# Kernel tuning notes

Hardware: AMD Instinct MI355X
Metric: run time of the kernel (lower is better)

## Reference

```python
import jax, jax.numpy as jnp
import numpy as np

B, T, H, NIN, D = 128, 64, 100, 3, 10


def _gru_cell(x, h, Wih, Whh, bih, bhh):
    # torch GRU cell: r,z,n gate ordering
    gi = x @ Wih.T + bih
    gh = h @ Whh.T + bhh
    ir, iz, inn = jnp.split(gi, 3, axis=-1)
    hr, hz, hn = jnp.split(gh, 3, axis=-1)
    r = jax.nn.sigmoid(ir + hr)
    z = jax.nn.sigmoid(iz + hz)
    n = jnp.tanh(inn + r * hn)
    return (1.0 - z) * n + z * h


def setup_inputs():
    keys = iter(jax.random.split(jax.random.key(0), 64))
    def rn(shape, scale):
        return jax.random.normal(next(keys), shape, dtype=jnp.float32) * scale
    inp = {"received": jax.random.normal(next(keys), (B, T, NIN), dtype=jnp.float32)}
    s = float(1.0 / np.sqrt(H))
    for p in ("w1", "w2"):
        inp[p + "_ih0"] = rn((3 * H, NIN), s)
        inp[p + "_hh0"] = rn((3 * H, H), s)
        inp[p + "_bih0"] = rn((3 * H,), s)
        inp[p + "_bhh0"] = rn((3 * H,), s)
        inp[p + "_ih1"] = rn((3 * H, H), s)
        inp[p + "_hh1"] = rn((3 * H, H), s)
        inp[p + "_bih1"] = rn((3 * H,), s)
        inp[p + "_bhh1"] = rn((3 * H,), s)
    s2 = float(1.0 / np.sqrt(2 * H))
    inp["attn_w"] = rn((1, 2 * H), s2)
    inp["attn_b"] = rn((1,), s2)
    inp["ctx_w"] = rn((H, 2 * H), s2)
    inp["ctx_b"] = rn((H,), s2)
    inp["out_w"] = rn((1, 2 * H), s2)
    inp["out_b"] = rn((1,), s2)
    return inp


def _forward(received, P1, P2, attn_w, attn_b, ctx_w, ctx_b, out_w, out_b):
    def two_layer(x, h, P):
        ih0, hh0, bih0, bhh0, ih1, hh1, bih1, bhh1 = P
        h0 = _gru_cell(x, h[0], ih0, hh0, bih0, bhh0)
        h1 = _gru_cell(h0, h[1], ih1, hh1, bih1, bhh1)
        # out = top-layer hidden; new hidden state [2,B,H]
        return h1, jnp.stack([h0, h1])

    def attend(hn, cache, t):
        # hn [2,B,H] (raw GRU hidden), cache [2,B,T,H] of past raw hiddens
        hrep = jnp.broadcast_to(hn[:, :, None, :], cache.shape)
        e = (jnp.concatenate([hrep, cache], axis=-1) @ attn_w.T)[..., 0] + attn_b[0]  # [2,B,T]
        mask = jnp.arange(T) < jnp.maximum(t, 1)  # safe mask (never all-False)
        a = jax.nn.softmax(jnp.where(mask, e, -1e30), axis=-1)
        c = jnp.einsum('lbt,lbth->lbh', a, cache)
        return jnp.concatenate([c, hn], axis=-1) @ ctx_w.T + ctx_b

    x_tm = jnp.transpose(received, (1, 0, 2))  # [T,B,NIN]
    h_init = jnp.zeros((2, B, H), jnp.float32)
    cache_init = jnp.zeros((2, B, T, H), jnp.float32)

    def step(carry, inp):
        h1, h2, c1, c2 = carry
        x, t = inp
        o1, h1n = two_layer(x, h1, P1)
        o2, h2n = two_layer(x, h2, P2)
        # attention over hiddens from steps 0..t-1 (cache updated AFTER attending)
        h1mix = attend(h1n, c1, t)
        h2mix = attend(h2n, c2, t)
        c1 = jax.lax.dynamic_update_slice(c1, h1n[:, :, None, :], (0, 0, t, 0))
        c2 = jax.lax.dynamic_update_slice(c2, h2n[:, :, None, :], (0, 0, t, 0))
        first = (t == 0)
        h1next = jnp.where(first, h1n, h1mix)
        h2next = jnp.where(first, h2n, h2mix)
        return (h1next, h2next, c1, c2), (o1, o2)

    _, (out1, out2) = jax.lax.scan(step, (h_init, h_init, cache_init, cache_init),
                                   (x_tm, jnp.arange(T)))
    out1 = jnp.transpose(out1, (1, 0, 2))  # [B,T,H]
    out2 = jnp.transpose(out2, (1, 0, 2))
    # readout: bit i pairs rnn_out1[i] with rnn_out2[min(i+D, T-1)]
    idx = jnp.minimum(jnp.arange(T) + D, T - 1)
    rnn_out = jnp.concatenate([out1, out2[:, idx, :]], axis=-1)  # [B,T,2H]
    logits = rnn_out @ out_w.T + out_b  # dec_act == 'linear'
    return jax.nn.sigmoid(logits)  # [B,T,1]


def reference(received, w1_ih0, w1_hh0, w1_bih0, w1_bhh0, w1_ih1, w1_hh1, w1_bih1, w1_bhh1,
              w2_ih0, w2_hh0, w2_bih0, w2_bhh0, w2_ih1, w2_hh1, w2_bih1, w2_bhh1,
              attn_w, attn_b, ctx_w, ctx_b, out_w, out_b):
    P1 = (w1_ih0, w1_hh0, w1_bih0, w1_bhh0, w1_ih1, w1_hh1, w1_bih1, w1_bhh1)
    P2 = (w2_ih0, w2_hh0, w2_bih0, w2_bhh0, w2_ih1, w2_hh1, w2_bih1, w2_bhh1)
    return _forward(received, P1, P2, attn_w, attn_b, ctx_w, ctx_b, out_w, out_b)
```

## Files before the change

kernel.cpp:

```cpp
#include <hip/hip_runtime.h>
#include <stdint.h>

#define H100 100
#define T64  64
#define NB   128
#define DLAG 10

#define OFF_HH0 0
#define OFF_IH1 30000
#define OFF_HH1 60000
#define OFF_CTX 90000
#define OFF_AWC 100000
#define OFF_OW  100050
#define OFF_P   100152

typedef _Float16 half2_t __attribute__((ext_vector_type(2)));
typedef __fp16   pk16x2  __attribute__((ext_vector_type(2)));

__device__ __forceinline__ float fdot2u(uint32_t a, uint32_t b, float c) {
#if __has_builtin(__builtin_amdgcn_fdot2)
    return __builtin_amdgcn_fdot2(__builtin_bit_cast(half2_t, a),
                                  __builtin_bit_cast(half2_t, b), c, false);
#else
    half2_t ha = __builtin_bit_cast(half2_t, a), hb = __builtin_bit_cast(half2_t, b);
    return c + (float)ha[0]*(float)hb[0] + (float)ha[1]*(float)hb[1];
#endif
}
__device__ __forceinline__ uint32_t pkrtz(float a, float b) {
    pk16x2 h = __builtin_amdgcn_cvt_pkrtz(a, b);
    return __builtin_bit_cast(uint32_t, h);
}
__device__ __forceinline__ uint32_t pk_rn(float a, float b) {
    half2_t h; h[0] = (_Float16)a; h[1] = (_Float16)b;
    return __builtin_bit_cast(uint32_t, h);
}
__device__ __forceinline__ float lo16(uint32_t u){ return (float)__builtin_bit_cast(half2_t,u)[0]; }
__device__ __forceinline__ float hi16(uint32_t u){ return (float)__builtin_bit_cast(half2_t,u)[1]; }
__device__ __forceinline__ float sigm(float x){ return 1.f/(1.f+__expf(-x)); }
__device__ __forceinline__ float tanhfast(float x){ return 1.f - 2.f/(1.f+__expf(2.f*x)); }
__device__ __forceinline__ float gru_el(float pr, float pz, float gin, float ghn, float hp) {
    float r = sigm(pr), z = sigm(pz);
    float n = tanhfast(gin + r*ghn);
    return (1.f - z)*n + z*hp;
}
__device__ __forceinline__ float wsum(float v){
    #pragma unroll
    for (int off = 32; off; off >>= 1) v += __shfl_xor(v, off);
    return v;
}
__device__ __forceinline__ float wmax(float v){
    #pragma unroll
    for (int off = 32; off; off >>= 1) v = fmaxf(v, __shfl_xor(v, off));
    return v;
}
__device__ __forceinline__ uint32_t rlane(uint32_t v, int lane){
    return (uint32_t)__builtin_amdgcn_readlane((int)v, lane);
}

struct SMem {
    alignas(16) uint32_t cache_t[2][50][66];
    alignas(16) float grz1[200];
    alignas(16) float gin1[100];
    alignas(16) float ghn1[100];
    alignas(16) float grz2[200];
    alignas(16) float gin2[100];
    alignas(16) float ghn2[100];
    alignas(16) float sv[2][64];
    alignas(16) float atile[2][64];
    alignas(16) uint32_t cpkq[2][64];
    alignas(16) float hmix0[104];
    alignas(16) float hmix1[104];
    alignas(16) float x[192];
};

__global__ void prep_pack(const float* __restrict__ w1hh0, const float* __restrict__ w2hh0,
                          const float* __restrict__ w1ih1, const float* __restrict__ w2ih1,
                          const float* __restrict__ w1hh1, const float* __restrict__ w2hh1,
                          const float* __restrict__ attw,  const float* __restrict__ ctxw,
                          const float* __restrict__ outw,  uint32_t* __restrict__ ws) {
    int g = blockIdx.x*blockDim.x + threadIdx.x;
    if (g < 30000) {
        int br = g/15000, idx = g%15000;
        int j = idx/50, kp = idx%50;
        const float* w = br ? w2hh0 : w1hh0;
        ws[OFF_HH0 + g] = pk_rn(w[j*H100+2*kp], w[j*H100+2*kp+1]);
    } else if (g < 60000) {
        int t2 = g-30000; int br = t2/15000, idx = t2%15000;
        int j = idx/50, kp = idx%50;
        const float* w = br ? w2ih1 : w1ih1;
        ws[OFF_IH1 + t2] = pk_rn(w[j*H100+2*kp], w[j*H100+2*kp+1]);
    } else if (g < 90000) {
        int t2 = g-60000; int br = t2/15000, idx = t2%15000;
        int j = idx/50, kp = idx%50;
        const float* w = br ? w2hh1 : w1hh1;
        ws[OFF_HH1 + t2] = pk_rn(w[j*H100+2*kp], w[j*H100+2*kp+1]);
    } else if (g < 100000) {
        int idx = g-90000; int o = idx/100, kp = idx%100;
        ws[OFF_CTX + idx] = pk_rn(ctxw[o*200+2*kp], ctxw[o*200+2*kp+1]);
    } else if (g < 100050) {
        int i2 = g-100000;
        ws[OFF_AWC + i2] = pk_rn(attw[100+2*i2], attw[101+2*i2]);
    } else if (g < 100150) {
        int t2 = g-100050; int br = t2/50, i2 = t2%50;
        ws[OFF_OW + t2] = pk_rn(outw[br*H100+2*i2], outw[br*H100+2*i2+1]);
    }
}

__global__ __launch_bounds__(512, 1)
void gru_seq(const float* __restrict__ recv,
             const float* __restrict__ ih0_1, const float* __restrict__ bih0_1,
             const float* __restrict__ bhh0_1, const float* __restrict__ bih1_1,
             const float* __restrict__ bhh1_1,
             const float* __restrict__ ih0_2, const float* __restrict__ bih0_2,
             const float* __restrict__ bhh0_2, const float* __restrict__ bih1_2,
             const float* __restrict__ bhh1_2,
             const float* __restrict__ ctxb,
             uint32_t* __restrict__ ws) {
    __shared__ SMem S;
    const int tid = threadIdx.x;
    const int w   = tid >> 6;
    const int la  = tid & 63;
    const int br  = blockIdx.x >> 7;
    const int b   = blockIdx.x & 127;

    const float* ih0 = br ? ih0_2  : ih0_1;
    const float* bi0 = br ? bih0_2 : bih0_1;
    const float* bh0 = br ? bhh0_2 : bhh0_1;
    const float* bi1 = br ? bih1_2 : bih1_1;
    const float* bh1 = br ? bhh1_2 : bhh1_1;

    for (int i = tid; i < 192; i += 512) S.x[i] = recv[b*192 + i];
    for (int i = tid; i < 2*50*66; i += 512) ((uint32_t*)S.cache_t)[i] = 0u;
    if (tid < 128) S.sv[tid>>6][tid&63] = 0.f;

    uint32_t wreg[150];
    float fb0=0.f, fb1=0.f, fb2=0.f, fb3=0.f;
    float rix0=0.f, rix1=0.f, rix2=0.f;
    if (tid < 300) {
        const uint32_t* p0 = ws + OFF_HH0 + br*15000 + tid*50;
        const uint32_t* p1 = ws + OFF_HH1 + br*15000 + tid*50;
        const uint32_t* p2 = ws + OFF_IH1 + br*15000 + tid*50;
        #pragma unroll
        for (int k = 0; k < 50; ++k) { wreg[k] = p0[k]; wreg[50+k] = p1[k]; wreg[100+k] = p2[k]; }
        fb0 = bi0[tid]; fb1 = bh0[tid]; fb2 = bi1[tid]; fb3 = bh1[tid];
        rix0 = ih0[tid*3]; rix1 = ih0[tid*3+1]; rix2 = ih0[tid*3+2];
    } else if (tid < 400) {
        const int o = tid - 300;
        const uint32_t* pc = ws + OFF_CTX + o*100;
        #pragma unroll
        for (int k = 0; k < 100; ++k) wreg[k] = pc[k];
        fb0 = ctxb[o];
    }
    uint32_t rawc = 0u, rowp = 0u;
    if (w == 0 && la < 50) rawc = ws[OFF_AWC + la];
    if (w == 7 && la < 50) rowp = ws[OFF_OW + br*50 + la];
    float* p_out = (float*)(ws + OFF_P);

    uint32_t hn0p = 0u, hn1p = 0u, h0cp = 0u, h1cp = 0u;
    float gh1save = 0.f;
    __syncthreads();

    for (int t = 0; t < T64; ++t) {
        if (la < 50) {
            if (t == 0)      { h0cp = 0u;   h1cp = 0u;   }
            else if (t == 1) { h0cp = hn0p; h1cp = hn1p; }
            else {
                float2 a0 = *(const float2*)&S.hmix0[2*la];
                float2 a1 = *(const float2*)&S.hmix1[2*la];
                h0cp = pkrtz(a0.x, a0.y);
                h1cp = pkrtz(a1.x, a1.y);
            }
        }
        if (tid < 300) {
            float x0 = S.x[3*t], x1 = S.x[3*t+1], x2 = S.x[3*t+2];
            float accI = fb0 + rix0*x0 + rix1*x1 + rix2*x2;
            float a0a = 0.f, a0b = 0.f;
            #pragma unroll
            for (int k = 0; k < 50; k += 2) {
                a0a = fdot2u(wreg[k],   rlane(h0cp, k),   a0a);
                a0b = fdot2u(wreg[k+1], rlane(h0cp, k+1), a0b);
            }
            float a1a = 0.f, a1b = 0.f;
            #pragma unroll
            for (int k = 0; k < 50; k += 2) {
                a1a = fdot2u(wreg[50+k],   rlane(h1cp, k),   a1a);
                a1b = fdot2u(wreg[50+k+1], rlane(h1cp, k+1), a1b);
            }
            float acc0 = fb1 + a0a + a0b;
            gh1save = fb3 + a1a + a1b;
            if (tid < 200) S.grz1[tid] = accI + acc0;
            else { S.gin1[tid-200] = accI; S.ghn1[tid-200] = acc0; }
        } else if (w == 5 || w == 6) {
            const int l = w - 5;
            const int m = (t > 1) ? t : 1;
            float sval = S.sv[l][la];
            float sv2  = (la < m) ? sval : -3e38f;
            float mx   = wmax(sv2);
            float p    = (la < m) ? __expf(sv2 - mx) : 0.f;
            float ssum = wsum(p);
            S.atile[l][la] = p;
            if (la < 50) {
                float c0 = 0.f, c1 = 0.f;
                const uint32_t* crow = &S.cache_t[l][la][0];
                const int np = (m + 1) >> 1;
                for (int tp = 0; tp < np; ++tp) {
                    float2 ap = *(const float2*)&S.atile[l][2*tp];
                    uint2  cp = *(const uint2*)&crow[2*tp];
                    c0 += ap.x*lo16(cp.x) + ap.y*lo16(cp.y);
                    c1 += ap.x*hi16(cp.x) + ap.y*hi16(cp.y);
                }
                float inv = 1.f/ssum;
                S.cpkq[l][la] = pkrtz(c0*inv, c1*inv);
            }
        } else if (w == 7 && t > 0) {
            float v = (la < 50) ? fdot2u(rowp, hn1p, 0.f) : 0.f;
            v = wsum(v);
            if (la == 0) p_out[br*8192 + b*64 + (t-1)] = v;
        }
        __syncthreads();
        if (la < 50) {
            float2 pr = *(const float2*)&S.grz1[2*la];
            float2 pz = *(const float2*)&S.grz1[100+2*la];
            float2 gi = *(const float2*)&S.gin1[2*la];
            float2 gh = *(const float2*)&S.ghn1[2*la];
            float h0 = gru_el(pr.x, pz.x, gi.x, gh.x, lo16(h0cp));
            float h1 = gru_el(pr.y, pz.y, gi.y, gh.y, hi16(h0cp));
            hn0p = pkrtz(h0, h1);
        }
        if (w == 0) {
            float v = (la < 50) ? fdot2u(rawc, hn0p, 0.f) : 0.f;
            v = wsum(v);
            if (la == 0) S.sv[0][t] = v;
            if (la < 50) S.cache_t[0][la][t] = hn0p;
        }
        if (tid < 300) {
            float ga = 0.f, gb = 0.f;
            #pragma unroll
            for (int k = 0; k < 50; k += 2) {
                ga = fdot2u(wreg[100+k],   rlane(hn0p, k),   ga);
                gb = fdot2u(wreg[100+k+1], rlane(hn0p, k+1), gb);
            }
            float gi1 = fb2 + ga + gb;
            if (tid < 200) S.grz2[tid] = gi1 + gh1save;
            else { S.gin2[tid-200] = gi1; S.ghn2[tid-200] = gh1save; }
        }
        __syncthreads();
        if (la < 50) {
            float2 pr = *(const float2*)&S.grz2[2*la];
            float2 pz = *(const float2*)&S.grz2[100+2*la];
            float2 gi = *(const float2*)&S.gin2[2*la];
            float2 gh = *(const float2*)&S.ghn2[2*la];
            float h0 = gru_el(pr.x, pz.x, gi.x, gh.x, lo16(h1cp));
            float h1 = gru_el(pr.y, pz.y, gi.y, gh.y, hi16(h1cp));
            hn1p = pkrtz(h0, h1);
        }
        if (w == 0) {
            float v = (la < 50) ? fdot2u(rawc, hn1p, 0.f) : 0.f;
            v = wsum(v);
            if (la == 0) S.sv[1][t] = v;
            if (la < 50) S.cache_t[1][la][t] = hn1p;
        }
        if (tid >= 300 && tid < 400) {
            const int o = tid - 300;
            float p0 = fb0, p1 = fb0;
            #pragma unroll
            for (int kb = 0; kb < 13; ++kb) {
                uint4 v0 = *(const uint4*)&S.cpkq[0][kb*4];
                uint4 v1 = *(const uint4*)&S.cpkq[1][kb*4];
                #pragma unroll
                for (int i = 0; i < 4; ++i) {
                    const int k = kb*4 + i;
                    if (k < 50) {
                        uint32_t e0 = (i==0)?v0.x:(i==1)?v0.y:(i==2)?v0.z:v0.w;
                        uint32_t e1 = (i==0)?v1.x:(i==1)?v1.y:(i==2)?v1.z:v1.w;
                        p0 = fdot2u(wreg[k], e0, p0);
                        p1 = fdot2u(wreg[k], e1, p1);
                    }
                }
            }
            #pragma unroll
            for (int k = 0; k < 50; ++k) {
                p0 = fdot2u(wreg[50+k], rlane(hn0p, k), p0);
                p1 = fdot2u(wreg[50+k], rlane(hn1p, k), p1);
            }
            S.hmix0[o] = p0; S.hmix1[o] = p1;
        }
        __syncthreads();
    }
    if (w == 7) {
        float v = (la < 50) ? fdot2u(rowp, hn1p, 0.f) : 0.f;
        v = wsum(v);
        if (la == 0) p_out[br*8192 + b*64 + 63] = v;
    }
}

__global__ void fin_out(const uint32_t* __restrict__ ws, const float* __restrict__ outb,
                        float* __restrict__ out) {
    int i = blockIdx.x*blockDim.x + threadIdx.x;
    if (i >= NB*T64) return;
    int b = i >> 6, t = i & 63;
    const float* p = (const float*)(ws + OFF_P);
    int t2 = t + DLAG; if (t2 > T64-1) t2 = T64-1;
    float logit = p[0*8192 + b*64 + t] + p[1*8192 + b*64 + t2] + outb[0];
    out[i] = 1.f/(1.f+__expf(-logit));
}

extern "C" void kernel_launch(void* const* d_in, const int* in_sizes, int n_in,
                              void* d_out, int out_size, void* d_ws, size_t ws_size,
                              hipStream_t stream) {
    const float* recv   = (const float*)d_in[0];
    const float* w1ih0  = (const float*)d_in[1];
    const float* w1hh0  = (const float*)d_in[2];
    const float* w1bih0 = (const float*)d_in[3];
    const float* w1bhh0 = (const float*)d_in[4];
    const float* w1ih1  = (const float*)d_in[5];
    const float* w1hh1  = (const float*)d_in[6];
    const float* w1bih1 = (const float*)d_in[7];
    const float* w1bhh1 = (const float*)d_in[8];
    const float* w2ih0  = (const float*)d_in[9];
    const float* w2hh0  = (const float*)d_in[10];
    const float* w2bih0 = (const float*)d_in[11];
    const float* w2bhh0 = (const float*)d_in[12];
    const float* w2ih1  = (const float*)d_in[13];
    const float* w2hh1  = (const float*)d_in[14];
    const float* w2bih1 = (const float*)d_in[15];
    const float* w2bhh1 = (const float*)d_in[16];
    const float* attw   = (const float*)d_in[17];
    const float* ctxw   = (const float*)d_in[19];
    const float* ctxb   = (const float*)d_in[20];
    const float* outw   = (const float*)d_in[21];
    const float* outb   = (const float*)d_in[22];
    uint32_t* ws = (uint32_t*)d_ws;
    float* out = (float*)d_out;

    prep_pack<<<(100150 + 255)/256, 256, 0, stream>>>(
        w1hh0, w2hh0, w1ih1, w2ih1, w1hh1, w2hh1, attw, ctxw, outw, ws);

    gru_seq<<<256, 512, 0, stream>>>(
        recv,
        w1ih0, w1bih0, w1bhh0, w1bih1, w1bhh1,
        w2ih0, w2bih0, w2bhh0, w2bih1, w2bhh1,
        ctxb, ws);

    fin_out<<<(NB*T64 + 255)/256, 256, 0, stream>>>(ws, outb, out);
}
```

Baseline: 263.8 us.

## Split GRU recurrent work across 768 threads and halve context projection per lane

Raises the block from 512 to 768 threads. A separate group of 300 threads now computes the layer-1 hidden-hidden matvec, which lets each thread hold 100 weight registers instead of 150. The context projection is split into two halves (attention context and raw hidden) spread over four waves, and the partial sums are added when the next step reads them. The output readout moves into the loop. The intent is to shorten the serial critical path of each timestep and to ease register pressure, at the cost of more waves contending for the CU and more LDS traffic.

```diff
diff --git a/kernel.cpp b/kernel.cpp
--- a/kernel.cpp
+++ b/kernel.cpp
@@ -60,16 +60,18 @@
 struct SMem {
     alignas(16) uint32_t cache_t[2][50][66];
     alignas(16) float grz1[200];
-    alignas(16) float gin1[100];
-    alignas(16) float ghn1[100];
+    alignas(16) float gin1[104];
+    alignas(16) float ghn1[104];
     alignas(16) float grz2[200];
-    alignas(16) float gin2[100];
-    alignas(16) float ghn2[100];
+    alignas(16) float gin2[104];
+    alignas(16) float gh1s[304];
     alignas(16) float sv[2][64];
     alignas(16) float atile[2][64];
     alignas(16) uint32_t cpkq[2][64];
-    alignas(16) float hmix0[104];
-    alignas(16) float hmix1[104];
+    alignas(16) float hmA0[104];
+    alignas(16) float hmA1[104];
+    alignas(16) float hmB0[104];
+    alignas(16) float hmB1[104];
     alignas(16) float x[192];
 };
 
@@ -106,7 +108,7 @@
     }
 }
 
-__global__ __launch_bounds__(512, 1)
+__global__ __launch_bounds__(768, 1)
 void gru_seq(const float* __restrict__ recv,
              const float* __restrict__ ih0_1, const float* __restrict__ bih0_1,
              const float* __restrict__ bhh0_1, const float* __restrict__ bih1_1,
@@ -129,35 +131,42 @@
     const float* bi1 = br ? bih1_2 : bih1_1;
     const float* bh1 = br ? bhh1_2 : bhh1_1;
 
-    for (int i = tid; i < 192; i += 512) S.x[i] = recv[b*192 + i];
-    for (int i = tid; i < 2*50*66; i += 512) ((uint32_t*)S.cache_t)[i] = 0u;
+    for (int i = tid; i < 192; i += 768) S.x[i] = recv[b*192 + i];
+    for (int i = tid; i < 2*50*66; i += 768) ((uint32_t*)S.cache_t)[i] = 0u;
     if (tid < 128) S.sv[tid>>6][tid&63] = 0.f;
 
-    uint32_t wreg[150];
-    float fb0=0.f, fb1=0.f, fb2=0.f, fb3=0.f;
+    uint32_t wreg[100];
+    float fbi0=0.f, fbh0=0.f, fbi1=0.f, fbh1=0.f, fbc=0.f;
     float rix0=0.f, rix1=0.f, rix2=0.f;
+    int co=0, chalf=0;
     if (tid < 300) {
         const uint32_t* p0 = ws + OFF_HH0 + br*15000 + tid*50;
-        const uint32_t* p1 = ws + OFF_HH1 + br*15000 + tid*50;
         const uint32_t* p2 = ws + OFF_IH1 + br*15000 + tid*50;
         #pragma unroll
-        for (int k = 0; k < 50; ++k) { wreg[k] = p0[k]; wreg[50+k] = p1[k]; wreg[100+k] = p2[k]; }
-        fb0 = bi0[tid]; fb1 = bh0[tid]; fb2 = bi1[tid]; fb3 = bh1[tid];
+        for (int k = 0; k < 50; ++k) { wreg[k] = p0[k]; wreg[50+k] = p2[k]; }
+        fbi0 = bi0[tid]; fbh0 = bh0[tid]; fbi1 = bi1[tid];
         rix0 = ih0[tid*3]; rix1 = ih0[tid*3+1]; rix2 = ih0[tid*3+2];
-    } else if (tid < 400) {
-        const int o = tid - 300;
-        const uint32_t* pc = ws + OFF_CTX + o*100;
+    } else if (tid >= 384 && tid < 684) {
+        const int r = tid - 384;
+        const uint32_t* p1 = ws + OFF_HH1 + br*15000 + r*50;
         #pragma unroll
-        for (int k = 0; k < 100; ++k) wreg[k] = pc[k];
-        fb0 = ctxb[o];
+        for (int k = 0; k < 50; ++k) wreg[k] = p1[k];
+        fbh1 = bh1[r];
+        if (w >= 6 && w <= 9 && la < 50) {
+            chalf = (w - 6) >> 1;
+            co    = ((w - 6) & 1)*50 + la;
+            const uint32_t* pc = ws + OFF_CTX + co*100 + chalf*50;
+            #pragma unroll
+            for (int k = 0; k < 50; ++k) wreg[50+k] = pc[k];
+            fbc = chalf ? 0.f : ctxb[co];
+        }
     }
     uint32_t rawc = 0u, rowp = 0u;
-    if (w == 0 && la < 50) rawc = ws[OFF_AWC + la];
-    if (w == 7 && la < 50) rowp = ws[OFF_OW + br*50 + la];
+    if ((w == 5 || w == 11) && la < 50) rawc = ws[OFF_AWC + la];
+    if (w == 5 && la < 50) rowp = ws[OFF_OW + br*50 + la];
     float* p_out = (float*)(ws + OFF_P);
 
     uint32_t hn0p = 0u, hn1p = 0u, h0cp = 0u, h1cp = 0u;
-    float gh1save = 0.f;
     __syncthreads();
 
     for (int t = 0; t < T64; ++t) {
@@ -165,33 +174,28 @@
             if (t == 0)      { h0cp = 0u;   h1cp = 0u;   }
             else if (t == 1) { h0cp = hn0p; h1cp = hn1p; }
             else {
-                float2 a0 = *(const float2*)&S.hmix0[2*la];
-                float2 a1 = *(const float2*)&S.hmix1[2*la];
-                h0cp = pkrtz(a0.x, a0.y);
-                h1cp = pkrtz(a1.x, a1.y);
+                float2 a0 = *(const float2*)&S.hmA0[2*la];
+                float2 b0 = *(const float2*)&S.hmB0[2*la];
+                float2 a1 = *(const float2*)&S.hmA1[2*la];
+                float2 b1 = *(const float2*)&S.hmB1[2*la];
+                h0cp = pkrtz(a0.x + b0.x, a0.y + b0.y);
+                h1cp = pkrtz(a1.x + b1.x, a1.y + b1.y);
             }
         }
         if (tid < 300) {
             float x0 = S.x[3*t], x1 = S.x[3*t+1], x2 = S.x[3*t+2];
-            float accI = fb0 + rix0*x0 + rix1*x1 + rix2*x2;
+            float accI = fbi0 + rix0*x0 + rix1*x1 + rix2*x2;
             float a0a = 0.f, a0b = 0.f;
             #pragma unroll
             for (int k = 0; k < 50; k += 2) {
                 a0a = fdot2u(wreg[k],   rlane(h0cp, k),   a0a);
                 a0b = fdot2u(wreg[k+1], rlane(h0cp, k+1), a0b);
             }
-            float a1a = 0.f, a1b = 0.f;
-            #pragma unroll
-            for (int k = 0; k < 50; k += 2) {
-                a1a = fdot2u(wreg[50+k],   rlane(h1cp, k),   a1a);
-                a1b = fdot2u(wreg[50+k+1], rlane(h1cp, k+1), a1b);
-            }
-            float acc0 = fb1 + a0a + a0b;
-            gh1save = fb3 + a1a + a1b;
+            float acc0 = fbh0 + a0a + a0b;
             if (tid < 200) S.grz1[tid] = accI + acc0;
             else { S.gin1[tid-200] = accI; S.ghn1[tid-200] = acc0; }
-        } else if (w == 5 || w == 6) {
-            const int l = w - 5;
+        } else if (w == 5 || w == 11) {
+            const int l = (w == 5) ? 0 : 1;
             const int m = (t > 1) ? t : 1;
             float sval = S.sv[l][la];
             float sv2  = (la < m) ? sval : -3e38f;
@@ -212,10 +216,15 @@
                 float inv = 1.f/ssum;
                 S.cpkq[l][la] = pkrtz(c0*inv, c1*inv);
             }
-        } else if (w == 7 && t > 0) {
-            float v = (la < 50) ? fdot2u(rowp, hn1p, 0.f) : 0.f;
-            v = wsum(v);
-            if (la == 0) p_out[br*8192 + b*64 + (t-1)] = v;
+        } else if (tid >= 384 && tid < 684) {
+            const int r = tid - 384;
+            float g1a = 0.f, g1b = 0.f;
+            #pragma unroll
+            for (int k = 0; k < 50; k += 2) {
+                g1a = fdot2u(wreg[k],   rlane(h1cp, k),   g1a);
+                g1b = fdot2u(wreg[k+1], rlane(h1cp, k+1), g1b);
+            }
+            S.gh1s[r] = fbh1 + g1a + g1b;
         }
         __syncthreads();
         if (la < 50) {
@@ -227,70 +236,74 @@
             float h1 = gru_el(pr.y, pz.y, gi.y, gh.y, hi16(h0cp));
             hn0p = pkrtz(h0, h1);
         }
-        if (w == 0) {
+        if (tid < 300) {
+            float ga = 0.f, gb = 0.f;
+            #pragma unroll
+            for (int k = 0; k < 50; k += 2) {
+                ga = fdot2u(wreg[50+k],   rlane(hn0p, k),   ga);
+                gb = fdot2u(wreg[50+k+1], rlane(hn0p, k+1), gb);
+            }
+            float gi1 = fbi1 + ga + gb;
+            if (tid < 200) S.grz2[tid] = gi1 + S.gh1s[tid];
+            else S.gin2[tid-200] = gi1;
+        }
+        if (w == 5) {
             float v = (la < 50) ? fdot2u(rawc, hn0p, 0.f) : 0.f;
             v = wsum(v);
             if (la == 0) S.sv[0][t] = v;
             if (la < 50) S.cache_t[0][la][t] = hn0p;
-        }
-        if (tid < 300) {
-            float ga = 0.f, gb = 0.f;
-            #pragma unroll
-            for (int k = 0; k < 50; k += 2) {
-                ga = fdot2u(wreg[100+k],   rlane(hn0p, k),   ga);
-                gb = fdot2u(wreg[100+k+1], rlane(hn0p, k+1), gb);
-            }
-            float gi1 = fb2 + ga + gb;
-            if (tid < 200) S.grz2[tid] = gi1 + gh1save;
-            else { S.gin2[tid-200] = gi1; S.ghn2[tid-200] = gh1save; }
         }
         __syncthreads();
         if (la < 50) {
             float2 pr = *(const float2*)&S.grz2[2*la];
             float2 pz = *(const float2*)&S.grz2[100+2*la];
             float2 gi = *(const float2*)&S.gin2[2*la];
-            float2 gh = *(const float2*)&S.ghn2[2*la];
+            float2 gh = *(const float2*)&S.gh1s[200+2*la];
             float h0 = gru_el(pr.x, pz.x, gi.x, gh.x, lo16(h1cp));
             float h1 = gru_el(pr.y, pz.y, gi.y, gh.y, hi16(h1cp));
             hn1p = pkrtz(h0, h1);
         }
-        if (w == 0) {
+        if (w >= 6 && w <= 9) {
+            if (la < 50) {
+                if (chalf == 0) {
+                    float p0 = fbc, p1 = fbc;
+                    #pragma unroll
+                    for (int kb = 0; kb < 13; ++kb) {
+                        uint4 v0 = *(const uint4*)&S.cpkq[0][kb*4];
+                        uint4 v1 = *(const uint4*)&S.cpkq[1][kb*4];
+                        #pragma unroll
+                        for (int i = 0; i < 4; ++i) {
+                            const int k = kb*4 + i;
+                            if (k < 50) {
+                                uint32_t e0 = (i==0)?v0.x:(i==1)?v0.y:(i==2)?v0.z:v0.w;
+                                uint32_t e1 = (i==0)?v1.x:(i==1)?v1.y:(i==2)?v1.z:v1.w;
+                                p0 = fdot2u(wreg[50+k], e0, p0);
+                                p1 = fdot2u(wreg[50+k], e1, p1);
+                            }
+                        }
+                    }
+                    S.hmA0[co] = p0; S.hmA1[co] = p1;
+                } else {
+                    float p0 = 0.f, p1 = 0.f;
+                    #pragma unroll
+                    for (int k = 0; k < 50; ++k) {
+                        p0 = fdot2u(wreg[50+k], rlane(hn0p, k), p0);
+                        p1 = fdot2u(wreg[50+k], rlane(hn1p, k), p1);
+                    }
+                    S.hmB0[co] = p0; S.hmB1[co] = p1;
+                }
+            }
+        } else if (w == 11) {
             float v = (la < 50) ? fdot2u(rawc, hn1p, 0.f) : 0.f;
             v = wsum(v);
             if (la == 0) S.sv[1][t] = v;
             if (la < 50) S.cache_t[1][la][t] = hn1p;
-        }
-        if (tid >= 300 && tid < 400) {
-            const int o = tid - 300;
-            float p0 = fb0, p1 = fb0;
-            #pragma unroll
-            for (int kb = 0; kb < 13; ++kb) {
-                uint4 v0 = *(const uint4*)&S.cpkq[0][kb*4];
-                uint4 v1 = *(const uint4*)&S.cpkq[1][kb*4];
-                #pragma unroll
-                for (int i = 0; i < 4; ++i) {
-                    const int k = kb*4 + i;
-                    if (k < 50) {
-                        uint32_t e0 = (i==0)?v0.x:(i==1)?v0.y:(i==2)?v0.z:v0.w;
-                        uint32_t e1 = (i==0)?v1.x:(i==1)?v1.y:(i==2)?v1.z:v1.w;
-                        p0 = fdot2u(wreg[k], e0, p0);
-                        p1 = fdot2u(wreg[k], e1, p1);
-                    }
-                }
-            }
-            #pragma unroll
-            for (int k = 0; k < 50; ++k) {
-                p0 = fdot2u(wreg[50+k], rlane(hn0p, k), p0);
-                p1 = fdot2u(wreg[50+k], rlane(hn1p, k), p1);
-            }
-            S.hmix0[o] = p0; S.hmix1[o] = p1;
+        } else if (w == 5) {
+            float v = (la < 50) ? fdot2u(rowp, hn1p, 0.f) : 0.f;
+            v = wsum(v);
+            if (la == 0) p_out[br*8192 + b*64 + t] = v;
         }
         __syncthreads();
-    }
-    if (w == 7) {
-        float v = (la < 50) ? fdot2u(rowp, hn1p, 0.f) : 0.f;
-        v = wsum(v);
-        if (la == 0) p_out[br*8192 + b*64 + 63] = v;
     }
 }
 
@@ -336,7 +349,7 @@
     prep_pack<<<(100150 + 255)/256, 256, 0, stream>>>(
         w1hh0, w2hh0, w1ih1, w2ih1, w1hh1, w2hh1, attw, ctxw, outw, ws);
 
-    gru_seq<<<256, 512, 0, stream>>>(
+    gru_seq<<<256, 768, 0, stream>>>(
         recv,
         w1ih0, w1bih0, w1bhh0, w1bih1, w1bhh1,
         w2ih0, w2bih0, w2bhh0, w2bih1, w2bhh1,
```

Result: slower. 270.9 us (+2.7%).

## Broadcast packed hidden states via LDS vector loads instead of readlane

Applied to the files above, without the earlier changes.

Replaces the per-element readlane broadcasts of packed hidden states with packed fp16 vectors stored in shared memory and read as uint4, and uses more independent dot-product accumulators. GRU elementwise updates move to the attention waves (5 and 6), the context projection packs its outputs directly into fp16 pairs via shuffle, and one extra barrier is added per stage. This is meant to cut the scalar readlane bottleneck and the dependency chains in the matvecs, at the cost of more barriers per timestep and more serialized work on two waves.

```diff
diff --git a/kernel.cpp b/kernel.cpp
--- a/kernel.cpp
+++ b/kernel.cpp
@@ -53,23 +53,22 @@
     for (int off = 32; off; off >>= 1) v = fmaxf(v, __shfl_xor(v, off));
     return v;
 }
-__device__ __forceinline__ uint32_t rlane(uint32_t v, int lane){
-    return (uint32_t)__builtin_amdgcn_readlane((int)v, lane);
-}
 
 struct SMem {
     alignas(16) uint32_t cache_t[2][50][66];
     alignas(16) float grz1[200];
-    alignas(16) float gin1[100];
-    alignas(16) float ghn1[100];
+    alignas(16) float gin1[104];
+    alignas(16) float ghn1[104];
     alignas(16) float grz2[200];
-    alignas(16) float gin2[100];
-    alignas(16) float ghn2[100];
+    alignas(16) float gin2[104];
+    alignas(16) float ghn2[104];
     alignas(16) float sv[2][64];
     alignas(16) float atile[2][64];
-    alignas(16) uint32_t cpkq[2][64];
-    alignas(16) float hmix0[104];
-    alignas(16) float hmix1[104];
+    alignas(16) uint32_t cpkq[2][52];
+    alignas(16) uint32_t h0c[52];
+    alignas(16) uint32_t h1c[52];
+    alignas(16) uint32_t hn0[52];
+    alignas(16) uint32_t hn1[52];
     alignas(16) float x[192];
 };
 
@@ -132,6 +131,8 @@
     for (int i = tid; i < 192; i += 512) S.x[i] = recv[b*192 + i];
     for (int i = tid; i < 2*50*66; i += 512) ((uint32_t*)S.cache_t)[i] = 0u;
     if (tid < 128) S.sv[tid>>6][tid&63] = 0.f;
+    if (tid < 104) { S.cpkq[0][tid>>1] = 0u; S.cpkq[1][tid>>1] = 0u; }
+    if (tid >= 128 && tid < 180) { int i2 = tid-128; S.h0c[i2]=0u; S.h1c[i2]=0u; S.hn0[i2]=0u; S.hn1[i2]=0u; }
 
     uint32_t wreg[150];
     float fb0=0.f, fb1=0.f, fb2=0.f, fb3=0.f;
@@ -152,42 +153,41 @@
         fb0 = ctxb[o];
     }
     uint32_t rawc = 0u, rowp = 0u;
-    if (w == 0 && la < 50) rawc = ws[OFF_AWC + la];
+    if ((w == 5 || w == 6) && la < 50) rawc = ws[OFF_AWC + la];
     if (w == 7 && la < 50) rowp = ws[OFF_OW + br*50 + la];
     float* p_out = (float*)(ws + OFF_P);
 
-    uint32_t hn0p = 0u, hn1p = 0u, h0cp = 0u, h1cp = 0u;
     float gh1save = 0.f;
     __syncthreads();
 
     for (int t = 0; t < T64; ++t) {
-        if (la < 50) {
-            if (t == 0)      { h0cp = 0u;   h1cp = 0u;   }
-            else if (t == 1) { h0cp = hn0p; h1cp = hn1p; }
-            else {
-                float2 a0 = *(const float2*)&S.hmix0[2*la];
-                float2 a1 = *(const float2*)&S.hmix1[2*la];
-                h0cp = pkrtz(a0.x, a0.y);
-                h1cp = pkrtz(a1.x, a1.y);
-            }
-        }
         if (tid < 300) {
             float x0 = S.x[3*t], x1 = S.x[3*t+1], x2 = S.x[3*t+2];
             float accI = fb0 + rix0*x0 + rix1*x1 + rix2*x2;
-            float a0a = 0.f, a0b = 0.f;
+            float a0=0.f,a1=0.f,a2=0.f,a3=0.f, b0=0.f,b1=0.f,b2=0.f,b3=0.f;
             #pragma unroll
-            for (int k = 0; k < 50; k += 2) {
-                a0a = fdot2u(wreg[k],   rlane(h0cp, k),   a0a);
-                a0b = fdot2u(wreg[k+1], rlane(h0cp, k+1), a0b);
-            }
-            float a1a = 0.f, a1b = 0.f;
-            #pragma unroll
-            for (int k = 0; k < 50; k += 2) {
-                a1a = fdot2u(wreg[50+k],   rlane(h1cp, k),   a1a);
-                a1b = fdot2u(wreg[50+k+1], rlane(h1cp, k+1), a1b);
-            }
-            float acc0 = fb1 + a0a + a0b;
-            gh1save = fb3 + a1a + a1b;
+            for (int i = 0; i < 12; ++i) {
+                uint4 h0 = *(const uint4*)&S.h0c[4*i];
+                uint4 h1 = *(const uint4*)&S.h1c[4*i];
+                a0 = fdot2u(wreg[4*i],    h0.x, a0);
+                b0 = fdot2u(wreg[50+4*i], h1.x, b0);
+                a1 = fdot2u(wreg[4*i+1],    h0.y, a1);
+                b1 = fdot2u(wreg[50+4*i+1], h1.y, b1);
+                a2 = fdot2u(wreg[4*i+2],    h0.z, a2);
+                b2 = fdot2u(wreg[50+4*i+2], h1.z, b2);
+                a3 = fdot2u(wreg[4*i+3],    h0.w, a3);
+                b3 = fdot2u(wreg[50+4*i+3], h1.w, b3);
+            }
+            {
+                uint2 h0t = *(const uint2*)&S.h0c[48];
+                uint2 h1t = *(const uint2*)&S.h1c[48];
+                a0 = fdot2u(wreg[48],    h0t.x, a0);
+                b0 = fdot2u(wreg[98],    h1t.x, b0);
+                a1 = fdot2u(wreg[49],    h0t.y, a1);
+                b1 = fdot2u(wreg[99],    h1t.y, b1);
+            }
+            float acc0 = fb1 + ((a0+a1)+(a2+a3));
+            gh1save    = fb3 + ((b0+b1)+(b2+b3));
             if (tid < 200) S.grz1[tid] = accI + acc0;
             else { S.gin1[tid-200] = accI; S.ghn1[tid-200] = acc0; }
         } else if (w == 5 || w == 6) {
@@ -203,92 +203,142 @@
                 float c0 = 0.f, c1 = 0.f;
                 const uint32_t* crow = &S.cache_t[l][la][0];
                 const int np = (m + 1) >> 1;
-                for (int tp = 0; tp < np; ++tp) {
-                    float2 ap = *(const float2*)&S.atile[l][2*tp];
-                    uint2  cp = *(const uint2*)&crow[2*tp];
-                    c0 += ap.x*lo16(cp.x) + ap.y*lo16(cp.y);
-                    c1 += ap.x*hi16(cp.x) + ap.y*hi16(cp.y);
+                for (int tb = 0; tb < np; tb += 8) {
+                    float2 ap[8]; uint2 cp[8];
+                    #pragma unroll
+                    for (int j = 0; j < 8; ++j) {
+                        ap[j] = *(const float2*)&S.atile[l][2*(tb+j)];
+                        cp[j] = *(const uint2*)&crow[2*(tb+j)];
+                    }
+                    #pragma unroll
+                    for (int j = 0; j < 8; ++j) {
+                        c0 += ap[j].x*lo16(cp[j].x) + ap[j].y*lo16(cp[j].y);
+                        c1 += ap[j].x*hi16(cp[j].x) + ap[j].y*hi16(cp[j].y);
+                    }
                 }
                 float inv = 1.f/ssum;
                 S.cpkq[l][la] = pkrtz(c0*inv, c1*inv);
             }
-        } else if (w == 7 && t > 0) {
-            float v = (la < 50) ? fdot2u(rowp, hn1p, 0.f) : 0.f;
-            v = wsum(v);
-            if (la == 0) p_out[br*8192 + b*64 + (t-1)] = v;
-        }
-        __syncthreads();
-        if (la < 50) {
-            float2 pr = *(const float2*)&S.grz1[2*la];
-            float2 pz = *(const float2*)&S.grz1[100+2*la];
-            float2 gi = *(const float2*)&S.gin1[2*la];
-            float2 gh = *(const float2*)&S.ghn1[2*la];
-            float h0 = gru_el(pr.x, pz.x, gi.x, gh.x, lo16(h0cp));
-            float h1 = gru_el(pr.y, pz.y, gi.y, gh.y, hi16(h0cp));
-            hn0p = pkrtz(h0, h1);
-        }
-        if (w == 0) {
+        }
+        __syncthreads();
+        if (w == 5) {
+            uint32_t hn0p = 0u;
+            if (la < 50) {
+                float2 pr = *(const float2*)&S.grz1[2*la];
+                float2 pz = *(const float2*)&S.grz1[100+2*la];
+                float2 gi = *(const float2*)&S.gin1[2*la];
+                float2 gh = *(const float2*)&S.ghn1[2*la];
+                uint32_t hp = S.h0c[la];
+                float h0 = gru_el(pr.x, pz.x, gi.x, gh.x, lo16(hp));
+                float h1 = gru_el(pr.y, pz.y, gi.y, gh.y, hi16(hp));
+                hn0p = pkrtz(h0, h1);
+                S.hn0[la] = hn0p;
+                S.cache_t[0][la][t] = hn0p;
+            }
             float v = (la < 50) ? fdot2u(rawc, hn0p, 0.f) : 0.f;
             v = wsum(v);
             if (la == 0) S.sv[0][t] = v;
-            if (la < 50) S.cache_t[0][la][t] = hn0p;
-        }
+        } else if (w == 7 && t > 0) {
+            float v = (la < 50) ? fdot2u(rowp, S.hn1[la], 0.f) : 0.f;
+            v = wsum(v);
+            if (la == 0) p_out[br*8192 + b*64 + (t-1)] = v;
+        }
+        __syncthreads();
         if (tid < 300) {
-            float ga = 0.f, gb = 0.f;
+            float g0=0.f,g1=0.f,g2=0.f,g3=0.f;
             #pragma unroll
-            for (int k = 0; k < 50; k += 2) {
-                ga = fdot2u(wreg[100+k],   rlane(hn0p, k),   ga);
-                gb = fdot2u(wreg[100+k+1], rlane(hn0p, k+1), gb);
-            }
-            float gi1 = fb2 + ga + gb;
+            for (int i = 0; i < 12; ++i) {
+                uint4 h = *(const uint4*)&S.hn0[4*i];
+                g0 = fdot2u(wreg[100+4*i],   h.x, g0);
+                g1 = fdot2u(wreg[100+4*i+1], h.y, g1);
+                g2 = fdot2u(wreg[100+4*i+2], h.z, g2);
+                g3 = fdot2u(wreg[100+4*i+3], h.w, g3);
+            }
+            {
+                uint2 ht = *(const uint2*)&S.hn0[48];
+                g0 = fdot2u(wreg[148], ht.x, g0);
+                g1 = fdot2u(wreg[149], ht.y, g1);
+            }
+            float gi1 = fb2 + ((g0+g1)+(g2+g3));
             if (tid < 200) S.grz2[tid] = gi1 + gh1save;
             else { S.gin2[tid-200] = gi1; S.ghn2[tid-200] = gh1save; }
         }
         __syncthreads();
-        if (la < 50) {
-            float2 pr = *(const float2*)&S.grz2[2*la];
-            float2 pz = *(const float2*)&S.grz2[100+2*la];
-            float2 gi = *(const float2*)&S.gin2[2*la];
-            float2 gh = *(const float2*)&S.ghn2[2*la];
-            float h0 = gru_el(pr.x, pz.x, gi.x, gh.x, lo16(h1cp));
-            float h1 = gru_el(pr.y, pz.y, gi.y, gh.y, hi16(h1cp));
-            hn1p = pkrtz(h0, h1);
-        }
-        if (w == 0) {
+        if (w == 6) {
+            uint32_t hn1p = 0u;
+            if (la < 50) {
+                float2 pr = *(const float2*)&S.grz2[2*la];
+                float2 pz = *(const float2*)&S.grz2[100+2*la];
+                float2 gi = *(const float2*)&S.gin2[2*la];
+                float2 gh = *(const float2*)&S.ghn2[2*la];
+                uint32_t hp = S.h1c[la];
+                float h0 = gru_el(pr.x, pz.x, gi.x, gh.x, lo16(hp));
+                float h1 = gru_el(pr.y, pz.y, gi.y, gh.y, hi16(hp));
+                hn1p = pkrtz(h0, h1);
+                S.hn1[la] = hn1p;
+                S.cache_t[1][la][t] = hn1p;
+            }
             float v = (la < 50) ? fdot2u(rawc, hn1p, 0.f) : 0.f;
             v = wsum(v);
             if (la == 0) S.sv[1][t] = v;
-            if (la < 50) S.cache_t[1][la][t] = hn1p;
-        }
+        }
+        __syncthreads();
         if (tid >= 300 && tid < 400) {
             const int o = tid - 300;
-            float p0 = fb0, p1 = fb0;
+            float p0a=fb0, p0b=0.f, q0a=0.f, q0b=0.f;
+            float p1a=fb0, p1b=0.f, q1a=0.f, q1b=0.f;
             #pragma unroll
-            for (int kb = 0; kb < 13; ++kb) {
-                uint4 v0 = *(const uint4*)&S.cpkq[0][kb*4];
-                uint4 v1 = *(const uint4*)&S.cpkq[1][kb*4];
-                #pragma unroll
-                for (int i = 0; i < 4; ++i) {
-                    const int k = kb*4 + i;
-                    if (k < 50) {
-                        uint32_t e0 = (i==0)?v0.x:(i==1)?v0.y:(i==2)?v0.z:v0.w;
-                        uint32_t e1 = (i==0)?v1.x:(i==1)?v1.y:(i==2)?v1.z:v1.w;
-                        p0 = fdot2u(wreg[k], e0, p0);
-                        p1 = fdot2u(wreg[k], e1, p1);
-                    }
-                }
-            }
-            #pragma unroll
-            for (int k = 0; k < 50; ++k) {
-                p0 = fdot2u(wreg[50+k], rlane(hn0p, k), p0);
-                p1 = fdot2u(wreg[50+k], rlane(hn1p, k), p1);
-            }
-            S.hmix0[o] = p0; S.hmix1[o] = p1;
+            for (int i = 0; i < 12; ++i) {
+                uint4 c0 = *(const uint4*)&S.cpkq[0][4*i];
+                uint4 c1 = *(const uint4*)&S.cpkq[1][4*i];
+                uint4 h0 = *(const uint4*)&S.hn0[4*i];
+                uint4 h1 = *(const uint4*)&S.hn1[4*i];
+                p0a = fdot2u(wreg[4*i],   c0.x, p0a);
+                p1a = fdot2u(wreg[4*i],   c1.x, p1a);
+                q0a = fdot2u(wreg[50+4*i],   h0.x, q0a);
+                q1a = fdot2u(wreg[50+4*i],   h1.x, q1a);
+                p0b = fdot2u(wreg[4*i+1], c0.y, p0b);
+                p1b = fdot2u(wreg[4*i+1], c1.y, p1b);
+                q0b = fdot2u(wreg[50+4*i+1], h0.y, q0b);
+                q1b = fdot2u(wreg[50+4*i+1], h1.y, q1b);
+                p0a = fdot2u(wreg[4*i+2], c0.z, p0a);
+                p1a = fdot2u(wreg[4*i+2], c1.z, p1a);
+                q0a = fdot2u(wreg[50+4*i+2], h0.z, q0a);
+                q1a = fdot2u(wreg[50+4*i+2], h1.z, q1a);
+                p0b = fdot2u(wreg[4*i+3], c0.w, p0b);
+                p1b = fdot2u(wreg[4*i+3], c1.w, p1b);
+                q0b = fdot2u(wreg[50+4*i+3], h0.w, q0b);
+                q1b = fdot2u(wreg[50+4*i+3], h1.w, q1b);
+            }
+            {
+                uint2 c0 = *(const uint2*)&S.cpkq[0][48];
+                uint2 c1 = *(const uint2*)&S.cpkq[1][48];
+                uint2 h0 = *(const uint2*)&S.hn0[48];
+                uint2 h1 = *(const uint2*)&S.hn1[48];
+                p0a = fdot2u(wreg[48], c0.x, p0a);
+                p1a = fdot2u(wreg[48], c1.x, p1a);
+                q0a = fdot2u(wreg[98], h0.x, q0a);
+                q1a = fdot2u(wreg[98], h1.x, q1a);
+                p0b = fdot2u(wreg[49], c0.y, p0b);
+                p1b = fdot2u(wreg[49], c1.y, p1b);
+                q0b = fdot2u(wreg[99], h0.y, q0b);
+                q1b = fdot2u(wreg[99], h1.y, q1b);
+            }
+            float m0 = (p0a+p0b) + (q0a+q0b);
+            float m1 = (p1a+p1b) + (q1a+q1b);
+            float n0 = __shfl_down(m0, 1);
+            float n1 = __shfl_down(m1, 1);
+            if (t > 0 && !(o & 1)) {
+                S.h0c[o>>1] = pkrtz(m0, n0);
+                S.h1c[o>>1] = pkrtz(m1, n1);
+            }
+        } else if (w == 7 && t == 0) {
+            if (la < 50) { S.h0c[la] = S.hn0[la]; S.h1c[la] = S.hn1[la]; }
         }
         __syncthreads();
     }
     if (w == 7) {
-        float v = (la < 50) ? fdot2u(rowp, hn1p, 0.f) : 0.f;
+        float v = (la < 50) ? fdot2u(rowp, S.hn1[la], 0.f) : 0.f;
         v = wsum(v);
         if (la == 0) p_out[br*8192 + b*64 + 63] = v;
     }
```

Result: faster. 227.0 us (-14.0%).
